# Kernel optimization log

Measured on AMD Instinct MI355X. Metric: run time of the kernel, lower is better.

## Reference

```python
import jax, jax.numpy as jnp
import numpy as np

N = 100000   # nodes
E = 1000000  # edges
H = 64       # hidden_channels
L = 3        # num_layers
B = 256      # graphs in batch
VOCAB = 100  # embedding table size


def _gru(m, h, wih, whh, bih, bhh):
    # torch.nn.GRUCell semantics, gate order r, z, n
    gi = m @ wih.T + bih            # [N, 3H]
    gh = h @ whh.T + bhh            # [N, 3H]
    ir, iz, inn = jnp.split(gi, 3, axis=-1)
    hr, hz, hn = jnp.split(gh, 3, axis=-1)
    r = jax.nn.sigmoid(ir + hr)
    z = jax.nn.sigmoid(iz + hz)
    n = jnp.tanh(inn + r * hn)
    return (1.0 - z) * n + z * h


def setup_inputs() -> dict:
    key = jax.random.key(0)
    ks = jax.random.split(key, 20)
    s = 1.0 / np.sqrt(H)
    inp = {
        "x": jax.random.randint(ks[0], (N, 1), 0, VOCAB),
        "edge_index": jax.random.randint(ks[1], (2, E), 0, N),
        "edge_attr": jax.random.uniform(ks[2], (E, 1), dtype=jnp.float32),
        "batch": jnp.sort(jax.random.randint(ks[3], (N,), 0, B)),
        "node_emb": jax.random.normal(ks[4], (VOCAB, H), jnp.float32),
        "edge_W": jax.random.normal(ks[5], (H, 1), jnp.float32) * s,
        "edge_b": jnp.zeros((H,), jnp.float32),
        "ggc_W": jax.random.normal(ks[6], (L, H, H), jnp.float32) * s,
        "gru_wih": jax.random.normal(ks[7], (L, 3 * H, H), jnp.float32) * s,
        "gru_whh": jax.random.normal(ks[8], (L, 3 * H, H), jnp.float32) * s,
        "gru_bih": jnp.zeros((L, 3 * H), jnp.float32),
        "gru_bhh": jnp.zeros((L, 3 * H), jnp.float32),
        "fc1_W": jax.random.normal(ks[9], (H // 2, H), jnp.float32) * s,
        "fc1_b": jnp.zeros((H // 2,), jnp.float32),
        "fc2_W": jax.random.normal(ks[10], (H // 4, H // 2), jnp.float32) * (1.0 / np.sqrt(H // 2)),
        "fc2_b": jnp.zeros((H // 4,), jnp.float32),
        "fc3_W": jax.random.normal(ks[11], (1, H // 4), jnp.float32) * (1.0 / np.sqrt(H // 4)),
        "fc3_b": jnp.zeros((1,), jnp.float32),
    }
    return inp


def reference(x, edge_index, edge_attr, batch, node_emb, edge_W, edge_b,
              ggc_W, gru_wih, gru_whh, gru_bih, gru_bhh,
              fc1_W, fc1_b, fc2_W, fc2_b, fc3_W, fc3_b):
    h = node_emb[x[:, 0]]                       # [N, H] node embedding
    _e = edge_attr @ edge_W.T + edge_b          # computed in original, unused by convs
    src, dst = edge_index[0], edge_index[1]
    for l in range(L):
        m = h @ ggc_W[l]                        # per-node linear transform
        agg = jax.ops.segment_sum(m[src], dst, num_segments=N)  # scatter-add to dst
        h = _gru(agg, h, gru_wih[l], gru_whh[l], gru_bih[l], gru_bhh[l])
        h = jax.nn.relu(h)                      # dropout = identity in eval
    sums = jax.ops.segment_sum(h, batch, num_segments=B)
    counts = jax.ops.segment_sum(jnp.ones((N, 1), h.dtype), batch, num_segments=B)
    pooled = sums / jnp.maximum(counts, 1.0)    # global_mean_pool
    y = jax.nn.relu(pooled @ fc1_W.T + fc1_b)
    y = jax.nn.relu(y @ fc2_W.T + fc2_b)
    y = y @ fc3_W.T + fc3_b
    return y[:, 0]                              # squeeze(-1) -> [B]
```

## Files before the change

### kernel.cpp

```cpp
#include <hip/hip_runtime.h>
#include <cstdint>

using h8v = __attribute__((ext_vector_type(8))) _Float16;
using h4v = __attribute__((ext_vector_type(4))) _Float16;
using f4v = __attribute__((ext_vector_type(4))) float;

__device__ __forceinline__ float sigmoidf_(float x) {
  return 1.0f / (1.0f + __expf(-x));
}
__device__ __forceinline__ float tanhf_(float x) {
  return 2.0f / (1.0f + __expf(-2.0f * x)) - 1.0f;
}

#define BN 256
#define BCAP 4096
#define NBMAX 1024

__global__ __launch_bounds__(256) void k_embed(const int* __restrict__ x,
                                               const float* __restrict__ emb,
                                               _Float16* __restrict__ h16a,
                                               _Float16* __restrict__ h16b,
                                               int* __restrict__ zbuf, int zwords,
                                               const int* __restrict__ dst,
                                               int* __restrict__ hist,
                                               int N, int E) {
  __shared__ int lh[NBMAX];
  int idx = blockIdx.x * 256 + threadIdx.x;
  if (idx < zwords) zbuf[idx] = 0;
  if (idx < (N + 1) * 64) {
    int i = idx >> 6, j = idx & 63;
    if (i < N) {
      h16a[idx] = (_Float16)emb[x[i] * 64 + j];
    } else {
      h16a[idx] = (_Float16)0.0f;
      h16b[idx] = (_Float16)0.0f;
    }
  }
  if (blockIdx.x < 512) {
    for (int i = threadIdx.x; i < NBMAX; i += 256) lh[i] = 0;
    __syncthreads();
    for (int e = blockIdx.x * 256 + threadIdx.x; e < E; e += 512 * 256)
      atomicAdd(&lh[dst[e] >> 8], 1);
    __syncthreads();
    for (int i = threadIdx.x; i < NBMAX; i += 256)
      if (lh[i]) atomicAdd(&hist[i], lh[i]);
  }
}

__global__ __launch_bounds__(1024) void k_bscan(const int* __restrict__ hist,
                                                int* __restrict__ bbase, int nb) {
  __shared__ int sc[NBMAX];
  int t = threadIdx.x;
  int v = (t < nb) ? hist[t] : 0;
  sc[t] = v;
  __syncthreads();
  for (int off = 1; off < NBMAX; off <<= 1) {
    int xx = (t >= off) ? sc[t - off] : 0;
    __syncthreads();
    sc[t] += xx;
    __syncthreads();
  }
  if (t <= nb) bbase[t] = sc[t] - v;
}

#define EPB 4096
__global__ __launch_bounds__(256) void k_scatter(const int* __restrict__ src,
                                                 const int* __restrict__ dst,
                                                 const int* __restrict__ bbase,
                                                 int* __restrict__ cursor,
                                                 unsigned* __restrict__ ebuf,
                                                 int E, int nb) {
  __shared__ int lh[NBMAX];
  __shared__ int lbase[NBMAX];
  for (int i = threadIdx.x; i < NBMAX; i += 256) lh[i] = 0;
  __syncthreads();
  const int e0 = blockIdx.x * EPB;
  const int e1 = min(e0 + EPB, E);
  for (int e = e0 + threadIdx.x; e < e1; e += 256) atomicAdd(&lh[dst[e] >> 8], 1);
  __syncthreads();
  for (int i = threadIdx.x; i < nb; i += 256) {
    int c = lh[i];
    lbase[i] = c ? (bbase[i] + atomicAdd(&cursor[i], c)) : 0;
    lh[i] = 0;
  }
  __syncthreads();
  for (int e = e0 + threadIdx.x; e < e1; e += 256) {
    int d = dst[e];
    int b = d >> 8;
    int off = atomicAdd(&lh[b], 1);
    ebuf[lbase[b] + off] = ((unsigned)(d & 255) << 20) | (unsigned)src[e];
  }
}

__global__ __launch_bounds__(256) void k_csr(const unsigned* __restrict__ ebuf,
                                             const int* __restrict__ bbase,
                                             int* __restrict__ padCur,
                                             int* __restrict__ rowp,
                                             int* __restrict__ rowe,
                                             int* __restrict__ ssrc, int N) {
  __shared__ unsigned se[BCAP];
  __shared__ int ss[BCAP];
  __shared__ int cnt[BN], pex[BN], sc[BN];
  __shared__ int sbase;
  const int b = blockIdx.x;
  const int t = threadIdx.x;
  const int nbeg = b * BN;
  const int ebeg = bbase[b];
  int ne = bbase[b + 1] - ebeg;
  if (ne > BCAP) ne = BCAP;
  for (int i = t; i < ne; i += 256) se[i] = ebuf[ebeg + i];
  cnt[t] = 0;
  __syncthreads();
  for (int i = t; i < ne; i += 256) atomicAdd(&cnt[se[i] >> 20], 1);
  __syncthreads();
  const int c = cnt[t];
  const int p = (c + 7) & ~7;
  sc[t] = p;
  __syncthreads();
  for (int off = 1; off < BN; off <<= 1) {
    int xx = (t >= off) ? sc[t - off] : 0;
    __syncthreads();
    sc[t] += xx;
    __syncthreads();
  }
  const int pexcl = sc[t] - p;
  const int P = sc[BN - 1];
  if (t == 0) sbase = atomicAdd(padCur, P);
  pex[t] = pexcl;
  cnt[t] = 0;
  __syncthreads();
  const int n = nbeg + t;
  if (n < N) {
    rowp[n] = sbase + pexcl;
    rowe[n] = sbase + pexcl + p;
  }
  for (int i = c; i < p; ++i) ss[pexcl + i] = N;
  for (int i = t; i < ne; i += 256) {
    unsigned e = se[i];
    int dL = e >> 20;
    int off = atomicAdd(&cnt[dL], 1);
    ss[pex[dL] + off] = (int)(e & 0xFFFFF);
  }
  __syncthreads();
  for (int i = t; i < P; i += 256) ssrc[sbase + i] = ss[i];
}

__global__ __launch_bounds__(256) void k_wpack3(const float* __restrict__ wih_all,
                                                const float* __restrict__ ggc_all,
                                                const float* __restrict__ whh_all,
                                                _Float16* __restrict__ Bp) {
  int l = blockIdx.x >> 4;
  int tid = (blockIdx.x & 15) * 256 + threadIdx.x;
  const float* wih = wih_all + (size_t)l * 192 * 64;
  const float* ggc = ggc_all + (size_t)l * 64 * 64;
  const float* whh = whh_all + (size_t)l * 192 * 64;
  int lane = tid & 63;
  int t = (tid >> 6) & 3;
  int wg = tid >> 8;
  int g = wg & 3, w = wg >> 2;
  int j = 16 * w + (lane & 15);
  int kbase = t * 32 + (lane >> 4) * 8;
  _Float16 hv[8];
#pragma unroll
  for (int i = 0; i < 8; ++i) {
    int k = kbase + i;
    float v = 0.0f;
    if (k < 64) {
      if (g < 3) {
        const float* a = wih + (size_t)(g * 64 + j) * 64;
        const float* bp = ggc + (size_t)k * 64;
        float s = 0.0f;
#pragma unroll
        for (int m = 0; m < 64; ++m) s += a[m] * bp[m];
        v = s;
      }
    } else {
      if (g != 2) {
        int row = (g == 3 ? 2 : g) * 64 + j;
        v = whh[(size_t)row * 64 + (k - 64)];
      }
    }
    hv[i] = (_Float16)v;
  }
  _Float16* o = Bp + (size_t)l * 32768 + (size_t)tid * 8;
#pragma unroll
  for (int i = 0; i < 8; ++i) o[i] = hv[i];
}

__device__ __forceinline__ h8v f32lds_to_h8(const float* __restrict__ p) {
  f4v x0 = *(const f4v*)p;
  f4v x1 = *(const f4v*)(p + 4);
  h8v r;
#pragma unroll
  for (int i = 0; i < 4; ++i) {
    r[i] = (_Float16)x0[i];
    r[4 + i] = (_Float16)x1[i];
  }
  return r;
}

#define FSTRIDE 68
#define HSTRIDE 72

__global__ __launch_bounds__(256, 4) void k_gfu(const _Float16* __restrict__ hin16,
                                                _Float16* __restrict__ hout16,
                                                const int* __restrict__ rowp,
                                                const int* __restrict__ rowe,
                                                const int* __restrict__ ssrc,
                                                const _Float16* __restrict__ Bp,
                                                const float* __restrict__ bih,
                                                const float* __restrict__ bhh,
                                                const int* __restrict__ batch,
                                                float* __restrict__ psum,
                                                float* __restrict__ pcnt,
                                                int N, int nTiles, int last) {
  __shared__ float aggLds[16 * FSTRIDE];
  __shared__ _Float16 hLds[16 * HSTRIDE];
  __shared__ _Float16 oLds[16 * HSTRIDE];
  const int lane = threadIdx.x & 63;
  const int w = threadIdx.x >> 6;
  const int r15 = lane & 15;
  const int kg8 = (lane >> 4) * 8;
  const int jj = w * 16 + r15;

  const float b_r = bih[jj] + bhh[jj];
  const float b_z = bih[64 + jj] + bhh[64 + jj];
  const float b_i = bih[128 + jj];
  const float b_h = bhh[128 + jj];

  h8v b0[4], b1[4], b2[2], b3[2];
#pragma unroll
  for (int t = 0; t < 4; ++t) {
    b0[t] = *(const h8v*)(Bp + ((size_t)((w * 4 + 0) * 4 + t) * 64 + lane) * 8);
    b1[t] = *(const h8v*)(Bp + ((size_t)((w * 4 + 1) * 4 + t) * 64 + lane) * 8);
  }
#pragma unroll
  for (int t = 0; t < 2; ++t) {
    b2[t] = *(const h8v*)(Bp + ((size_t)((w * 4 + 2) * 4 + t) * 64 + lane) * 8);
    b3[t] = *(const h8v*)(Bp + ((size_t)((w * 4 + 3) * 4 + (2 + t)) * 64 + lane) * 8);
  }

  for (int tile = blockIdx.x; tile < nTiles; tile += gridDim.x) {
    const int n0 = tile * 16;
    __syncthreads();
    {
      const int g = lane >> 4;
      const int node = 4 * w + g;
      const int n = n0 + node;
      const int nc = min(n, N - 1);
      h4v hv = *(const h4v*)(hin16 + (size_t)nc * 64 + 4 * r15);
      f4v a0 = {0, 0, 0, 0}, a1 = {0, 0, 0, 0}, a2 = {0, 0, 0, 0}, a3 = {0, 0, 0, 0};
      if (n < N) {
        int e = rowp[n];
        const int end = rowe[n];
        if (e < end) {
          int i0 = ssrc[e], i1 = ssrc[e + 1], i2 = ssrc[e + 2], i3 = ssrc[e + 3];
          int i4 = ssrc[e + 4], i5 = ssrc[e + 5], i6 = ssrc[e + 6], i7 = ssrc[e + 7];
          do {
            const int ne = e + 8;
            h4v v0 = *(const h4v*)(hin16 + (size_t)i0 * 64 + 4 * r15);
            h4v v1 = *(const h4v*)(hin16 + (size_t)i1 * 64 + 4 * r15);
            h4v v2 = *(const h4v*)(hin16 + (size_t)i2 * 64 + 4 * r15);
            h4v v3 = *(const h4v*)(hin16 + (size_t)i3 * 64 + 4 * r15);
            h4v v4 = *(const h4v*)(hin16 + (size_t)i4 * 64 + 4 * r15);
            h4v v5 = *(const h4v*)(hin16 + (size_t)i5 * 64 + 4 * r15);
            h4v v6 = *(const h4v*)(hin16 + (size_t)i6 * 64 + 4 * r15);
            h4v v7 = *(const h4v*)(hin16 + (size_t)i7 * 64 + 4 * r15);
            if (ne < end) {
              i0 = ssrc[ne]; i1 = ssrc[ne + 1]; i2 = ssrc[ne + 2]; i3 = ssrc[ne + 3];
              i4 = ssrc[ne + 4]; i5 = ssrc[ne + 5]; i6 = ssrc[ne + 6]; i7 = ssrc[ne + 7];
            }
            a0 += __builtin_convertvector(v0, f4v);
            a1 += __builtin_convertvector(v1, f4v);
            a2 += __builtin_convertvector(v2, f4v);
            a3 += __builtin_convertvector(v3, f4v);
            a0 += __builtin_convertvector(v4, f4v);
            a1 += __builtin_convertvector(v5, f4v);
            a2 += __builtin_convertvector(v6, f4v);
            a3 += __builtin_convertvector(v7, f4v);
            e = ne;
          } while (e < end);
        }
      }
      a0 += a1; a2 += a3; a0 += a2;
      *(f4v*)(aggLds + node * FSTRIDE + 4 * r15) = a0;
      *(h4v*)(hLds + node * HSTRIDE + 4 * r15) = hv;
    }
    __syncthreads();

    h8v ah[4];
#pragma unroll
    for (int t = 0; t < 2; ++t)
      ah[t] = f32lds_to_h8(aggLds + r15 * FSTRIDE + t * 32 + kg8);
#pragma unroll
    for (int t = 0; t < 2; ++t)
      ah[2 + t] = *(const h8v*)(hLds + r15 * HSTRIDE + t * 32 + kg8);

    f4v acc0 = {0, 0, 0, 0}, acc1 = {0, 0, 0, 0}, acc2 = {0, 0, 0, 0}, acc3 = {0, 0, 0, 0};
#pragma unroll
    for (int t = 0; t < 4; ++t) {
      acc0 = __builtin_amdgcn_mfma_f32_16x16x32_f16(ah[t], b0[t], acc0, 0, 0, 0);
      acc1 = __builtin_amdgcn_mfma_f32_16x16x32_f16(ah[t], b1[t], acc1, 0, 0, 0);
    }
    acc2 = __builtin_amdgcn_mfma_f32_16x16x32_f16(ah[0], b2[0], acc2, 0, 0, 0);
    acc2 = __builtin_amdgcn_mfma_f32_16x16x32_f16(ah[1], b2[1], acc2, 0, 0, 0);
    acc3 = __builtin_amdgcn_mfma_f32_16x16x32_f16(ah[2], b3[0], acc3, 0, 0, 0);
    acc3 = __builtin_amdgcn_mfma_f32_16x16x32_f16(ah[3], b3[1], acc3, 0, 0, 0);

    const int rb = (lane >> 4) * 4;
#pragma unroll
    for (int q = 0; q < 4; ++q) {
      int row = rb + q;
      float hold = (float)hLds[row * HSTRIDE + jj];
      float r = sigmoidf_(acc0[q] + b_r);
      float z = sigmoidf_(acc1[q] + b_z);
      float nv = tanhf_(acc2[q] + b_i + r * (acc3[q] + b_h));
      float o = (1.0f - z) * nv + z * hold;
      oLds[row * HSTRIDE + jj] = (_Float16)fmaxf(o, 0.0f);
    }
    __syncthreads();

    if (!last) {
      const int node = threadIdx.x >> 4;
      const int ci = (threadIdx.x & 15) * 4;
      const int n = n0 + node;
      if (n < N) {
        h4v o = *(const h4v*)(oLds + node * HSTRIDE + ci);
        *(h4v*)(hout16 + (size_t)n * 64 + ci) = o;
      }
    } else {
      if (threadIdx.x < 64) {
        int curb = batch[n0];
        float acc = 0.0f, ca = 0.0f;
#pragma unroll 1
        for (int i = 0; i < 16; ++i) {
          int n = n0 + i;
          if (n >= N) break;
          int b = batch[n];
          if (b != curb) {
            atomicAdd(&psum[curb * 64 + lane], acc);
            if (lane == 0) atomicAdd(&pcnt[curb], ca);
            acc = 0.0f; ca = 0.0f; curb = b;
          }
          acc += (float)oLds[i * HSTRIDE + lane];
          ca += 1.0f;
        }
        atomicAdd(&psum[curb * 64 + lane], acc);
        if (lane == 0) atomicAdd(&pcnt[curb], ca);
      }
    }
  }
}

__global__ __launch_bounds__(64) void k_head(const float* __restrict__ psum,
                                             const float* __restrict__ pcnt,
                                             const float* __restrict__ fc1W,
                                             const float* __restrict__ fc1b,
                                             const float* __restrict__ fc2W,
                                             const float* __restrict__ fc2b,
                                             const float* __restrict__ fc3W,
                                             const float* __restrict__ fc3b,
                                             float* __restrict__ out) {
  int b = blockIdx.x;
  int j = threadIdx.x;
  float c = fmaxf(pcnt[b], 1.0f);
  float p = psum[b * 64 + j] / c;
  int j1 = j & 31;
  float y1 = fc1b[j1];
#pragma unroll
  for (int k = 0; k < 64; ++k) y1 += fc1W[j1 * 64 + k] * __shfl(p, k, 64);
  y1 = fmaxf(y1, 0.0f);
  int j2 = j & 15;
  float y2 = fc2b[j2];
#pragma unroll
  for (int k = 0; k < 32; ++k) y2 += fc2W[j2 * 32 + k] * __shfl(y1, k, 64);
  y2 = fmaxf(y2, 0.0f);
  float y = 0.0f;
#pragma unroll
  for (int k = 0; k < 16; ++k) y += fc3W[k] * __shfl(y2, k, 64);
  if (j == 0) out[b] = y + fc3b[0];
}

extern "C" void kernel_launch(void* const* d_in, const int* in_sizes, int n_in,
                              void* d_out, int out_size, void* d_ws, size_t ws_size,
                              hipStream_t stream) {
  const int N = in_sizes[0];
  const int E = in_sizes[1] / 2;
  const int B = out_size;

  const int* x = (const int*)d_in[0];
  const int* eidx = (const int*)d_in[1];
  const int* batch = (const int*)d_in[3];
  const float* emb = (const float*)d_in[4];
  const float* ggcW = (const float*)d_in[7];
  const float* wih = (const float*)d_in[8];
  const float* whh = (const float*)d_in[9];
  const float* bih = (const float*)d_in[10];
  const float* bhh = (const float*)d_in[11];
  const float* fc1W = (const float*)d_in[12];
  const float* fc1b = (const float*)d_in[13];
  const float* fc2W = (const float*)d_in[14];
  const float* fc2b = (const float*)d_in[15];
  const float* fc3W = (const float*)d_in[16];
  const float* fc3b = (const float*)d_in[17];
  float* out = (float*)d_out;

  const int* srcp = eidx;
  const int* dstp = eidx + E;
  const int nb = (N + BN - 1) / BN;

  char* ws = (char*)d_ws;
  size_t off = 0;
  auto alloc = [&](size_t bytes) -> void* {
    void* p = ws + off;
    off = (off + bytes + 255) & ~(size_t)255;
    return p;
  };
  _Float16* h16a = (_Float16*)alloc((size_t)(N + 1) * 64 * 2);
  _Float16* h16b = (_Float16*)alloc((size_t)(N + 1) * 64 * 2);
  int* rowp = (int*)alloc((size_t)(N + 1) * 4);
  int* rowe = (int*)alloc((size_t)(N + 1) * 4);
  int* ssrc = (int*)alloc(((size_t)E + 8 * (size_t)N) * 4);
  unsigned* ebuf = (unsigned*)alloc((size_t)E * 4);
  int* bbase = (int*)alloc((size_t)(NBMAX + 1) * 4);
  size_t zbeg = off;
  int* hist = (int*)alloc((size_t)NBMAX * 4);
  int* cursor = (int*)alloc((size_t)NBMAX * 4);
  int* padCur = (int*)alloc(256);
  float* pool = (float*)alloc((size_t)(B * 64 + B) * 4);
  size_t zend = off;
  float* psum = pool;
  float* pcnt = pool + (size_t)B * 64;
  _Float16* Bp = (_Float16*)alloc((size_t)3 * 32768 * 2);
  const int zwords = (int)((zend - zbeg) / 4);

  hipMemsetAsync(hist, 0, (size_t)NBMAX * 4, stream);
  k_embed<<<((N + 1) * 64 + 255) / 256, 256, 0, stream>>>(
      x, emb, h16a, h16b, (int*)(ws + zbeg + NBMAX * 4), zwords - NBMAX, dstp,
      hist, N, E);
  k_bscan<<<1, 1024, 0, stream>>>(hist, bbase, nb);
  k_scatter<<<(E + EPB - 1) / EPB, 256, 0, stream>>>(srcp, dstp, bbase, cursor,
                                                     ebuf, E, nb);
  k_csr<<<nb, 256, 0, stream>>>(ebuf, bbase, padCur, rowp, rowe, ssrc, N);
  k_wpack3<<<48, 256, 0, stream>>>(wih, ggcW, whh, Bp);

  const int nTiles = (N + 15) / 16;
  const int grid = nTiles < 2048 ? nTiles : 2048;
  _Float16* hh[2] = {h16a, h16b};
  for (int l = 0; l < 3; ++l) {
    int a = l & 1, b = 1 - a;
    k_gfu<<<grid, 256, 0, stream>>>(hh[a], hh[b], rowp, rowe, ssrc,
                                    Bp + (size_t)l * 32768,
                                    bih + (size_t)l * 192, bhh + (size_t)l * 192,
                                    batch, psum, pcnt, N, nTiles, l == 2 ? 1 : 0);
  }

  k_head<<<B, 64, 0, stream>>>(psum, pcnt, fc1W, fc1b, fc2W, fc2b, fc3W, fc3b, out);
}
```

Before: 203.2 us.

## Fold block scan into scatter/csr kernels and weight packing into embed kernel

Removes the standalone single-block prefix-scan kernel: each scatter block now recomputes the bucket base offsets from the histogram itself, and each CSR block reduces the histogram prefix to find its edge start. The weight-packing kernel is merged into the embedding kernel as extra blocks. This cuts two kernel launches and their serialization gaps, at the cost of redundant scan/reduction work in every scatter and CSR block.

```diff
diff --git a/kernel.cpp b/kernel.cpp
--- a/kernel.cpp
+++ b/kernel.cpp
@@ -23,6 +23,10 @@
                                                int* __restrict__ zbuf, int zwords,
                                                const int* __restrict__ dst,
                                                int* __restrict__ hist,
+                                               const float* __restrict__ wih_all,
+                                               const float* __restrict__ ggc_all,
+                                               const float* __restrict__ whh_all,
+                                               _Float16* __restrict__ Bp,
                                                int N, int E) {
   __shared__ int lh[NBMAX];
   int idx = blockIdx.x * 256 + threadIdx.x;
@@ -44,56 +48,96 @@
     __syncthreads();
     for (int i = threadIdx.x; i < NBMAX; i += 256)
       if (lh[i]) atomicAdd(&hist[i], lh[i]);
-  }
-}
-
-__global__ __launch_bounds__(1024) void k_bscan(const int* __restrict__ hist,
-                                                int* __restrict__ bbase, int nb) {
-  __shared__ int sc[NBMAX];
-  int t = threadIdx.x;
-  int v = (t < nb) ? hist[t] : 0;
-  sc[t] = v;
-  __syncthreads();
-  for (int off = 1; off < NBMAX; off <<= 1) {
-    int xx = (t >= off) ? sc[t - off] : 0;
-    __syncthreads();
-    sc[t] += xx;
-    __syncthreads();
-  }
-  if (t <= nb) bbase[t] = sc[t] - v;
+  } else if (blockIdx.x < 560) {
+    int wb = blockIdx.x - 512;
+    int l = wb >> 4;
+    int tid = (wb & 15) * 256 + threadIdx.x;
+    const float* wih = wih_all + (size_t)l * 192 * 64;
+    const float* ggc = ggc_all + (size_t)l * 64 * 64;
+    const float* whh = whh_all + (size_t)l * 192 * 64;
+    int lane = tid & 63;
+    int t = (tid >> 6) & 3;
+    int wg = tid >> 8;
+    int g = wg & 3, w = wg >> 2;
+    int j = 16 * w + (lane & 15);
+    int kbase = t * 32 + (lane >> 4) * 8;
+    _Float16 hv[8];
+#pragma unroll
+    for (int i = 0; i < 8; ++i) {
+      int k = kbase + i;
+      float v = 0.0f;
+      if (k < 64) {
+        if (g < 3) {
+          const float* a = wih + (size_t)(g * 64 + j) * 64;
+          const float* bp = ggc + (size_t)k * 64;
+          float s = 0.0f;
+#pragma unroll
+          for (int m = 0; m < 64; ++m) s += a[m] * bp[m];
+          v = s;
+        }
+      } else {
+        if (g != 2) {
+          int row = (g == 3 ? 2 : g) * 64 + j;
+          v = whh[(size_t)row * 64 + (k - 64)];
+        }
+      }
+      hv[i] = (_Float16)v;
+    }
+    _Float16* o = Bp + (size_t)l * 32768 + (size_t)tid * 8;
+#pragma unroll
+    for (int i = 0; i < 8; ++i) o[i] = hv[i];
+  }
 }
 
 #define EPB 4096
 __global__ __launch_bounds__(256) void k_scatter(const int* __restrict__ src,
                                                  const int* __restrict__ dst,
-                                                 const int* __restrict__ bbase,
+                                                 const int* __restrict__ hist,
                                                  int* __restrict__ cursor,
                                                  unsigned* __restrict__ ebuf,
                                                  int E, int nb) {
   __shared__ int lh[NBMAX];
-  __shared__ int lbase[NBMAX];
-  for (int i = threadIdx.x; i < NBMAX; i += 256) lh[i] = 0;
+  __shared__ int sbb[NBMAX];
+  __shared__ int tmp[256];
+  const int t = threadIdx.x;
+  int h0 = hist[4 * t], h1 = hist[4 * t + 1], h2 = hist[4 * t + 2], h3 = hist[4 * t + 3];
+  int s = h0 + h1 + h2 + h3;
+  tmp[t] = s;
+  __syncthreads();
+  for (int off = 1; off < 256; off <<= 1) {
+    int xx = (t >= off) ? tmp[t - off] : 0;
+    __syncthreads();
+    tmp[t] += xx;
+    __syncthreads();
+  }
+  int excl = tmp[t] - s;
+  sbb[4 * t] = excl;
+  sbb[4 * t + 1] = excl + h0;
+  sbb[4 * t + 2] = excl + h0 + h1;
+  sbb[4 * t + 3] = excl + h0 + h1 + h2;
+  for (int i = t; i < NBMAX; i += 256) lh[i] = 0;
   __syncthreads();
   const int e0 = blockIdx.x * EPB;
   const int e1 = min(e0 + EPB, E);
-  for (int e = e0 + threadIdx.x; e < e1; e += 256) atomicAdd(&lh[dst[e] >> 8], 1);
-  __syncthreads();
-  for (int i = threadIdx.x; i < nb; i += 256) {
+  for (int e = e0 + t; e < e1; e += 256) atomicAdd(&lh[dst[e] >> 8], 1);
+  __syncthreads();
+  for (int i = t; i < nb; i += 256) {
     int c = lh[i];
-    lbase[i] = c ? (bbase[i] + atomicAdd(&cursor[i], c)) : 0;
-    lh[i] = 0;
-  }
-  __syncthreads();
-  for (int e = e0 + threadIdx.x; e < e1; e += 256) {
+    if (c) lh[i] = sbb[i] + atomicAdd(&cursor[i], c);
+  }
+  __syncthreads();
+  for (int i = t; i < NBMAX; i += 256) sbb[i] = 0;
+  __syncthreads();
+  for (int e = e0 + t; e < e1; e += 256) {
     int d = dst[e];
     int b = d >> 8;
-    int off = atomicAdd(&lh[b], 1);
-    ebuf[lbase[b] + off] = ((unsigned)(d & 255) << 20) | (unsigned)src[e];
+    int off = atomicAdd(&sbb[b], 1);
+    ebuf[lh[b] + off] = ((unsigned)(d & 255) << 20) | (unsigned)src[e];
   }
 }
 
 __global__ __launch_bounds__(256) void k_csr(const unsigned* __restrict__ ebuf,
-                                             const int* __restrict__ bbase,
+                                             const int* __restrict__ hist,
                                              int* __restrict__ padCur,
                                              int* __restrict__ rowp,
                                              int* __restrict__ rowe,
@@ -101,12 +145,21 @@
   __shared__ unsigned se[BCAP];
   __shared__ int ss[BCAP];
   __shared__ int cnt[BN], pex[BN], sc[BN];
+  __shared__ int red[256];
   __shared__ int sbase;
   const int b = blockIdx.x;
   const int t = threadIdx.x;
   const int nbeg = b * BN;
-  const int ebeg = bbase[b];
-  int ne = bbase[b + 1] - ebeg;
+  int local = 0;
+  for (int i = t; i < b; i += 256) local += hist[i];
+  red[t] = local;
+  __syncthreads();
+  for (int off = 128; off > 0; off >>= 1) {
+    if (t < off) red[t] += red[t + off];
+    __syncthreads();
+  }
+  const int ebeg = red[0];
+  int ne = hist[b];
   if (ne > BCAP) ne = BCAP;
   for (int i = t; i < ne; i += 256) se[i] = ebuf[ebeg + i];
   cnt[t] = 0;
@@ -143,48 +196,6 @@
   }
   __syncthreads();
   for (int i = t; i < P; i += 256) ssrc[sbase + i] = ss[i];
-}
-
-__global__ __launch_bounds__(256) void k_wpack3(const float* __restrict__ wih_all,
-                                                const float* __restrict__ ggc_all,
-                                                const float* __restrict__ whh_all,
-                                                _Float16* __restrict__ Bp) {
-  int l = blockIdx.x >> 4;
-  int tid = (blockIdx.x & 15) * 256 + threadIdx.x;
-  const float* wih = wih_all + (size_t)l * 192 * 64;
-  const float* ggc = ggc_all + (size_t)l * 64 * 64;
-  const float* whh = whh_all + (size_t)l * 192 * 64;
-  int lane = tid & 63;
-  int t = (tid >> 6) & 3;
-  int wg = tid >> 8;
-  int g = wg & 3, w = wg >> 2;
-  int j = 16 * w + (lane & 15);
-  int kbase = t * 32 + (lane >> 4) * 8;
-  _Float16 hv[8];
-#pragma unroll
-  for (int i = 0; i < 8; ++i) {
-    int k = kbase + i;
-    float v = 0.0f;
-    if (k < 64) {
-      if (g < 3) {
-        const float* a = wih + (size_t)(g * 64 + j) * 64;
-        const float* bp = ggc + (size_t)k * 64;
-        float s = 0.0f;
-#pragma unroll
-        for (int m = 0; m < 64; ++m) s += a[m] * bp[m];
-        v = s;
-      }
-    } else {
-      if (g != 2) {
-        int row = (g == 3 ? 2 : g) * 64 + j;
-        v = whh[(size_t)row * 64 + (k - 64)];
-      }
-    }
-    hv[i] = (_Float16)v;
-  }
-  _Float16* o = Bp + (size_t)l * 32768 + (size_t)tid * 8;
-#pragma unroll
-  for (int i = 0; i < 8; ++i) o[i] = hv[i];
 }
 
 __device__ __forceinline__ h8v f32lds_to_h8(const float* __restrict__ p) {
@@ -422,9 +433,8 @@
   int* rowe = (int*)alloc((size_t)(N + 1) * 4);
   int* ssrc = (int*)alloc(((size_t)E + 8 * (size_t)N) * 4);
   unsigned* ebuf = (unsigned*)alloc((size_t)E * 4);
-  int* bbase = (int*)alloc((size_t)(NBMAX + 1) * 4);
+  int* hist = (int*)alloc((size_t)NBMAX * 4);
   size_t zbeg = off;
-  int* hist = (int*)alloc((size_t)NBMAX * 4);
   int* cursor = (int*)alloc((size_t)NBMAX * 4);
   int* padCur = (int*)alloc(256);
   float* pool = (float*)alloc((size_t)(B * 64 + B) * 4);
@@ -436,13 +446,11 @@
 
   hipMemsetAsync(hist, 0, (size_t)NBMAX * 4, stream);
   k_embed<<<((N + 1) * 64 + 255) / 256, 256, 0, stream>>>(
-      x, emb, h16a, h16b, (int*)(ws + zbeg + NBMAX * 4), zwords - NBMAX, dstp,
-      hist, N, E);
-  k_bscan<<<1, 1024, 0, stream>>>(hist, bbase, nb);
-  k_scatter<<<(E + EPB - 1) / EPB, 256, 0, stream>>>(srcp, dstp, bbase, cursor,
+      x, emb, h16a, h16b, (int*)(ws + zbeg), zwords, dstp, hist,
+      wih, ggcW, whh, Bp, N, E);
+  k_scatter<<<(E + EPB - 1) / EPB, 256, 0, stream>>>(srcp, dstp, hist, cursor,
                                                      ebuf, E, nb);
-  k_csr<<<nb, 256, 0, stream>>>(ebuf, bbase, padCur, rowp, rowe, ssrc, N);
-  k_wpack3<<<48, 256, 0, stream>>>(wih, ggcW, whh, Bp);
+  k_csr<<<nb, 256, 0, stream>>>(ebuf, hist, padCur, rowp, rowe, ssrc, N);
 
   const int nTiles = (N + 15) / 16;
   const int grid = nTiles < 2048 ? nTiles : 2048;
```

Result: faster. 195.4 us (-3.8%).
